# Kernel tuning notes

Measured on AMD Instinct MI355X. Metric: run time of the kernel, lower is better.

The kernel has to match this reference:

```python
import jax, jax.numpy as jnp
import numpy as np

B = 32768
N_TABLES = 26
N_ROWS = 200000
D = 64
N_DENSE = 13
NUM_PAIRS = (N_TABLES + 1) * N_TABLES // 2  # 351, pairs j < i over 27 vectors


def setup_inputs() -> dict:
    key = jax.random.key(0)
    ks = jax.random.split(key, 16)
    def lin(kw, kb, m, n):
        W = jax.random.normal(kw, (m, n), jnp.float32) * np.sqrt(2.0 / (m + n))
        b = jax.random.normal(kb, (m,), jnp.float32) * np.sqrt(1.0 / m)
        return W, b
    bw0, bb0 = lin(ks[0], ks[1], 512, N_DENSE)
    bw1, bb1 = lin(ks[2], ks[3], 256, 512)
    bw2, bb2 = lin(ks[4], ks[5], D, 256)
    tw0, tb0 = lin(ks[6], ks[7], 512, D + NUM_PAIRS)
    tw1, tb1 = lin(ks[8], ks[9], 256, 512)
    tw2, tb2 = lin(ks[10], ks[11], 1, 256)
    bound = np.sqrt(1.0 / N_ROWS)
    emb_tables = jax.random.uniform(ks[12], (N_TABLES, N_ROWS, D), jnp.float32,
                                    minval=-bound, maxval=bound)
    dense_x = jax.random.uniform(ks[13], (B, N_DENSE), jnp.float32)
    indices = jax.random.randint(ks[14], (N_TABLES, B), 0, N_ROWS, jnp.int64)
    return {"dense_x": dense_x, "indices": indices, "emb_tables": emb_tables,
            "bw0": bw0, "bb0": bb0, "bw1": bw1, "bb1": bb1, "bw2": bw2, "bb2": bb2,
            "tw0": tw0, "tb0": tb0, "tw1": tw1, "tb1": tb1, "tw2": tw2, "tb2": tb2}


def reference(dense_x, indices, emb_tables,
              bw0, bb0, bw1, bb1, bw2, bb2,
              tw0, tb0, tw1, tb1, tw2, tb2):
    # bottom MLP (all ReLU, sigmoid_bot = -1)
    h = jax.nn.relu(dense_x @ bw0.T + bb0)
    h = jax.nn.relu(h @ bw1.T + bb1)
    x_bot = jax.nn.relu(h @ bw2.T + bb2)          # [B, D]

    # multi-table EmbeddingBag(sum) with single-index bags -> plain gather
    embs = jax.vmap(lambda tbl, idx: tbl[idx])(emb_tables, indices)  # [26, B, D]

    # dot interaction over 27 feature vectors
    T = jnp.concatenate([x_bot[None], embs], axis=0).transpose(1, 0, 2)  # [B, 27, D]
    Z = jnp.einsum('bnd,bmd->bnm', T, T)                                 # [B, 27, 27]
    li, lj = jnp.tril_indices(N_TABLES + 1, k=-1)  # pairs with j < i (no self)
    Zflat = Z[:, li, lj]                           # [B, 351]
    R = jnp.concatenate([x_bot, Zflat], axis=1)    # [B, 415]

    # top MLP: ReLU, ReLU, Sigmoid (sigmoid_top = 2)
    h = jax.nn.relu(R @ tw0.T + tb0)
    h = jax.nn.relu(h @ tw1.T + tb1)
    p = jax.nn.sigmoid(h @ tw2.T + tb2)            # [B, 1]
    return p
```

## Files before the change

### kernel.cpp

```cpp
#include <hip/hip_runtime.h>
#include <cstddef>
#include <cstdint>

#define B_SZ    32768
#define NTAB    26
#define NROWS   200000

typedef __attribute__((ext_vector_type(8))) short short8v;
typedef __attribute__((ext_vector_type(4))) float f32x4;
typedef __attribute__((ext_vector_type(16))) float f32x16;

__device__ __forceinline__ ushort f2bf(float f) {
    uint32_t u = __builtin_bit_cast(uint32_t, f);
    u += 0x7FFFu + ((u >> 16) & 1u);
    return (ushort)(u >> 16);
}
__device__ __forceinline__ void stage16(const ushort* g, ushort* l) {
    __builtin_amdgcn_global_load_lds(
        (const __attribute__((address_space(1))) unsigned int*)g,
        (__attribute__((address_space(3))) unsigned int*)l, 16, 0, 0);
}
__device__ __forceinline__ void wait_stage_then_barrier(bool last) {
    if (last) asm volatile("s_waitcnt vmcnt(0)" ::: "memory");
    else      asm volatile("s_waitcnt vmcnt(4)" ::: "memory");
    __builtin_amdgcn_sched_barrier(0);
    __builtin_amdgcn_s_barrier();
    __builtin_amdgcn_sched_barrier(0);
}
__device__ __forceinline__ void reads_done_barrier() {
    __builtin_amdgcn_sched_barrier(0);
    __builtin_amdgcn_s_barrier();
    __builtin_amdgcn_sched_barrier(0);
}

__global__ __launch_bounds__(256) void conv_all_k(
    const float* __restrict__ dense_x, const float* __restrict__ bw0,
    const float* __restrict__ tw0, const float* __restrict__ bw1,
    const float* __restrict__ bw2, const float* __restrict__ tw1,
    ushort* __restrict__ dense_pad, ushort* __restrict__ bw0p,
    ushort* __restrict__ tw0p, ushort* __restrict__ bw1c,
    ushort* __restrict__ bw2c, ushort* __restrict__ tw1c)
{
    const int gid = blockIdx.x * 256 + threadIdx.x;
    if (gid < 1048576) {
        int r = gid >> 5, k = gid & 31;
        dense_pad[gid] = (k < 13) ? f2bf(dense_x[r * 13 + k]) : (ushort)0;
    } else if (gid < 1064960) {
        int i = gid - 1048576; int r = i >> 5, k = i & 31;
        bw0p[i] = (k < 13) ? f2bf(bw0[r * 13 + k]) : (ushort)0;
    } else if (gid < 1277952) {
        int i = gid - 1064960; int r = i / 416, k = i - r * 416;
        tw0p[i] = (k < 415) ? f2bf(tw0[r * 415 + k]) : (ushort)0;
    } else if (gid < 1409024) {
        int i = gid - 1277952; bw1c[i] = f2bf(bw1[i]);
    } else if (gid < 1425408) {
        int i = gid - 1409024; bw2c[i] = f2bf(bw2[i]);
    } else if (gid < 1556480) {
        int i = gid - 1425408; tw1c[i] = f2bf(tw1[i]);
    }
}

__global__ __launch_bounds__(256, 2) void fused_k(
    const ushort* __restrict__ dense_pad, const ushort* __restrict__ bw0p,
    const float* __restrict__ bb0, const ushort* __restrict__ bw1c,
    const float* __restrict__ bb1, const ushort* __restrict__ bw2c,
    const float* __restrict__ bb2,
    const float* __restrict__ emb, const int* __restrict__ indices,
    const ushort* __restrict__ tw0p, const float* __restrict__ tb0,
    const ushort* __restrict__ tw1c, const float* __restrict__ tb1,
    const float* __restrict__ tw2, const float* __restrict__ tb2,
    float* __restrict__ out)
{
    __shared__ __align__(16) ushort R1[32 * 512];
    __shared__ __align__(16) ushort Wst[2][256 * 32];
    __shared__ __align__(16) ushort R3[32 * 256];
    ushort* const Wf = &Wst[0][0];
    const int t = threadIdx.x;
    const int lane = t & 63, w = t >> 6;
    const int fr = lane & 15, j16 = lane >> 4;
    const int bBase = blockIdx.x * 32;

    int ir0, ir1, ir2, ir3;
    ir0 = indices[(size_t)(t >> 5) * B_SZ + bBase + (t & 31)];
    ir1 = indices[(size_t)((256 + t) >> 5) * B_SZ + bBase + ((256 + t) & 31)];
    ir2 = indices[(size_t)((512 + t) >> 5) * B_SZ + bBase + ((512 + t) & 31)];
    ir3 = (t < 64) ? indices[(size_t)((768 + t) >> 5) * B_SZ + bBase + ((768 + t) & 31)] : 0;

    if (t < 128) {
        const int r = t >> 2, u = t & 3, us = u ^ ((r >> 1) & 3);
        stage16(dense_pad + (size_t)(bBase + r) * 32 + us * 8, &R3[t * 8]);
    }
#pragma unroll
    for (int i = 0; i < 4; ++i) {
        const int idx = i * 256 + t;
        const int r = idx >> 2, u = idx & 3, us = u ^ ((r >> 1) & 3);
        stage16(bw0p + (size_t)r * 32 + us * 8, &Wst[0][idx * 8]);
        stage16(bw0p + (size_t)(256 + r) * 32 + us * 8, &Wst[1][idx * 8]);
    }
    __syncthreads();

    f32x4 acc0[2][2][4] = {};
    {
        short8v a[2];
#pragma unroll
        for (int m = 0; m < 2; ++m) {
            const int r = m * 16 + fr;
            a[m] = *(const short8v*)&R3[r * 32 + (j16 ^ ((r >> 1) & 3)) * 8];
        }
#pragma unroll
        for (int hh = 0; hh < 2; ++hh) {
            short8v b[4];
#pragma unroll
            for (int n = 0; n < 4; ++n) {
                const int lr = w * 64 + n * 16 + fr;
                b[n] = *(const short8v*)&Wst[hh][lr * 32 + (j16 ^ ((lr >> 1) & 3)) * 8];
            }
            __builtin_amdgcn_s_setprio(1);
#pragma unroll
            for (int m = 0; m < 2; ++m)
#pragma unroll
                for (int n = 0; n < 4; ++n)
                    acc0[hh][m][n] = __builtin_amdgcn_mfma_f32_16x16x32_bf16(b[n], a[m], acc0[hh][m][n], 0, 0, 0);
            __builtin_amdgcn_s_setprio(0);
        }
    }
    __syncthreads();

#pragma unroll
    for (int i = 0; i < 4; ++i) {
        const int idx = i * 256 + t;
        const int r = idx >> 2, u = idx & 3, us = u ^ ((r >> 1) & 3);
        stage16(bw1c + (size_t)r * 512 + us * 8, &Wst[0][idx * 8]);
        stage16(bw1c + (size_t)r * 512 + 32 + us * 8, &Wst[1][idx * 8]);
    }
#pragma unroll
    for (int hh = 0; hh < 2; ++hh)
#pragma unroll
    for (int n = 0; n < 4; ++n) {
        const int ch = hh * 256 + w * 64 + n * 16 + j16 * 4;
        const float4 bv = *(const float4*)&bb0[ch];
#pragma unroll
        for (int m = 0; m < 2; ++m) {
            const int s = m * 16 + fr;
            ushort4 o;
            o.x = f2bf(fmaxf(acc0[hh][m][n][0] + bv.x, 0.f));
            o.y = f2bf(fmaxf(acc0[hh][m][n][1] + bv.y, 0.f));
            o.z = f2bf(fmaxf(acc0[hh][m][n][2] + bv.z, 0.f));
            o.w = f2bf(fmaxf(acc0[hh][m][n][3] + bv.w, 0.f));
            const int u = ch >> 3, su = u ^ (s & 7);
            *(ushort4*)&R1[s * 512 + su * 8 + (ch & 7)] = o;
        }
    }
    __syncthreads();

    f32x4 acc1[2][4] = {};
    for (int st = 0; st < 16; ++st) {
        wait_stage_then_barrier(st == 15);
        const int kt = st * 32;
        short8v a[2], b[4];
#pragma unroll
        for (int m = 0; m < 2; ++m) {
            const int s = m * 16 + fr;
            const int u = (kt >> 3) + j16, su = u ^ (s & 7);
            a[m] = *(const short8v*)&R1[s * 512 + su * 8];
        }
#pragma unroll
        for (int n = 0; n < 4; ++n) {
            const int lr = w * 64 + n * 16 + fr;
            b[n] = *(const short8v*)&Wst[st & 1][lr * 32 + (j16 ^ ((lr >> 1) & 3)) * 8];
        }
        __builtin_amdgcn_s_setprio(1);
#pragma unroll
        for (int m = 0; m < 2; ++m)
#pragma unroll
            for (int n = 0; n < 4; ++n)
                acc1[m][n] = __builtin_amdgcn_mfma_f32_16x16x32_bf16(b[n], a[m], acc1[m][n], 0, 0, 0);
        __builtin_amdgcn_s_setprio(0);
        reads_done_barrier();
        if (st + 2 < 16) {
            const int kt2 = (st + 2) * 32;
#pragma unroll
            for (int i = 0; i < 4; ++i) {
                const int idx = i * 256 + t;
                const int r = idx >> 2, u = idx & 3, us = u ^ ((r >> 1) & 3);
                stage16(bw1c + (size_t)r * 512 + kt2 + us * 8, &Wst[st & 1][idx * 8]);
            }
        }
    }
#pragma unroll
    for (int i = 0; i < 8; ++i) {
        const int idx = i * 256 + t;
        const int st = idx >> 8, within = idx & 255;
        const int r = within >> 2, u = within & 3, us = u ^ ((r >> 1) & 3);
        stage16(bw2c + (size_t)r * 256 + st * 32 + us * 8, &Wf[idx * 8]);
    }
#pragma unroll
    for (int n = 0; n < 4; ++n) {
        const int ch = w * 64 + n * 16 + j16 * 4;
        const float4 bv = *(const float4*)&bb1[ch];
#pragma unroll
        for (int m = 0; m < 2; ++m) {
            const int s = m * 16 + fr;
            ushort4 o;
            o.x = f2bf(fmaxf(acc1[m][n][0] + bv.x, 0.f));
            o.y = f2bf(fmaxf(acc1[m][n][1] + bv.y, 0.f));
            o.z = f2bf(fmaxf(acc1[m][n][2] + bv.z, 0.f));
            o.w = f2bf(fmaxf(acc1[m][n][3] + bv.w, 0.f));
            const int u = ch >> 3, su = u ^ (s & 7);
            *(ushort4*)&R3[s * 256 + su * 8 + (ch & 7)] = o;
        }
    }
    __syncthreads();

    f32x4 acc2[2] = {};
    for (int kt = 0; kt < 256; kt += 32) {
        short8v a[2], b;
#pragma unroll
        for (int m = 0; m < 2; ++m) {
            const int s = m * 16 + fr;
            const int u = (kt >> 3) + j16, su = u ^ (s & 7);
            a[m] = *(const short8v*)&R3[s * 256 + su * 8];
        }
        {
            const int lr = w * 16 + fr;
            b = *(const short8v*)&Wf[(kt >> 5) * 2048 + lr * 32 + (j16 ^ ((lr >> 1) & 3)) * 8];
        }
#pragma unroll
        for (int m = 0; m < 2; ++m)
            acc2[m] = __builtin_amdgcn_mfma_f32_16x16x32_bf16(b, a[m], acc2[m], 0, 0, 0);
    }
    __syncthreads();

#pragma unroll
    for (int i = 0; i < 4; ++i) {
        const int idx = i * 256 + t;
        const int r = idx >> 2, u = idx & 3, us = u ^ ((r >> 1) & 3);
        stage16(tw0p + (size_t)r * 416 + us * 8, &Wst[0][idx * 8]);
        stage16(tw0p + (size_t)(256 + r) * 416 + us * 8, &Wst[1][idx * 8]);
    }
    {
        const int ch = w * 16 + j16 * 4;
        const float4 bv = *(const float4*)&bb2[ch];
#pragma unroll
        for (int m = 0; m < 2; ++m) {
            const int s = m * 16 + fr;
            ushort4 o;
            o.x = f2bf(fmaxf(acc2[m][0] + bv.x, 0.f));
            o.y = f2bf(fmaxf(acc2[m][1] + bv.y, 0.f));
            o.z = f2bf(fmaxf(acc2[m][2] + bv.z, 0.f));
            o.w = f2bf(fmaxf(acc2[m][3] + bv.w, 0.f));
            *(ushort4*)&R1[s * 424 + ch] = o;
        }
    }
    if (t < 32) R1[t * 424 + 415] = 0;
    {
        int* sc = (int*)R3;
        sc[t] = ir0; sc[256 + t] = ir1; sc[512 + t] = ir2;
        if (t < 64) sc[768 + t] = ir3;
    }
    __syncthreads();

    {
        const int* sc = (const int*)R3;
        const int r32 = lane & 31, half = lane >> 5;
        const bool isEmb = (r32 >= 1) && (r32 <= 26);
        const size_t tblOfs = isEmb ? (size_t)(r32 - 1) * NROWS : 0;

#define LOADRAW(dst, s_) { \
        const int idxv = isEmb ? sc[(r32 - 1) * 32 + (s_)] : 0; \
        const float* rp = emb + (tblOfs + (size_t)idxv) * 64 + half * 8; \
        _Pragma("unroll") \
        for (int kq = 0; kq < 4; ++kq) { \
            dst[2 * kq]     = *(const f32x4*)&rp[kq * 16]; \
            dst[2 * kq + 1] = *(const f32x4*)&rp[kq * 16 + 4]; } }

#define COMPUTE(raw, s_) { \
        short8v tf[4]; \
        _Pragma("unroll") \
        for (int kq = 0; kq < 4; ++kq) { \
            short8v v; \
            v[0] = (short)f2bf(raw[2 * kq][0]);     v[1] = (short)f2bf(raw[2 * kq][1]); \
            v[2] = (short)f2bf(raw[2 * kq][2]);     v[3] = (short)f2bf(raw[2 * kq][3]); \
            v[4] = (short)f2bf(raw[2 * kq + 1][0]); v[5] = (short)f2bf(raw[2 * kq + 1][1]); \
            v[6] = (short)f2bf(raw[2 * kq + 1][2]); v[7] = (short)f2bf(raw[2 * kq + 1][3]); \
            if (r32 == 0) v = *(const short8v*)&R1[(s_) * 424 + kq * 16 + half * 8]; \
            else if (!isEmb) v = (short8v)0; \
            tf[kq] = v; } \
        f32x16 c = {}; \
        _Pragma("unroll") \
        for (int kq = 0; kq < 4; ++kq) \
            c = __builtin_amdgcn_mfma_f32_32x32x16_bf16(tf[kq], tf[kq], c, 0, 0, 0); \
        _Pragma("unroll") \
        for (int reg = 0; reg < 16; ++reg) { \
            const int r = (reg & 3) + 8 * (reg >> 2) + 4 * half; \
            if (r < 27 && r32 < r) \
                R1[(s_) * 424 + 64 + (r * (r - 1)) / 2 + r32] = f2bf(c[reg]); } }

        f32x4 rawA[8], rawB[8];
        LOADRAW(rawA, w);
#pragma unroll
        for (int p = 0; p < 4; ++p) {
            const int sA = p * 8 + w;
            const int sB = p * 8 + 4 + w;
            LOADRAW(rawB, sB);
            COMPUTE(rawA, sA);
            if (p < 3) LOADRAW(rawA, p * 8 + 8 + w);
            COMPUTE(rawB, sB);
        }
#undef LOADRAW
#undef COMPUTE
    }
    __syncthreads();

    f32x4 accA[2][2][4] = {};
    for (int st = 0; st < 26; ++st) {
        wait_stage_then_barrier(st == 25);
        const int kt = (st >> 1) * 32, hh = st & 1;
        short8v a[2], b[4];
#pragma unroll
        for (int m = 0; m < 2; ++m) {
            const int s = m * 16 + fr;
            a[m] = *(const short8v*)&R1[s * 424 + ((kt >> 3) + j16) * 8];
        }
#pragma unroll
        for (int n = 0; n < 4; ++n) {
            const int lr = w * 64 + n * 16 + fr;
            b[n] = *(const short8v*)&Wst[st & 1][lr * 32 + (j16 ^ ((lr >> 1) & 3)) * 8];
        }
        __builtin_amdgcn_s_setprio(1);
#pragma unroll
        for (int m = 0; m < 2; ++m)
#pragma unroll
            for (int n = 0; n < 4; ++n)
                accA[hh][m][n] = __builtin_amdgcn_mfma_f32_16x16x32_bf16(b[n], a[m], accA[hh][m][n], 0, 0, 0);
        __builtin_amdgcn_s_setprio(0);
        reads_done_barrier();
        if (st + 2 < 26) {
            const int st2 = st + 2;
            const int kt2 = (st2 >> 1) * 32, hh2 = st2 & 1;
#pragma unroll
            for (int i = 0; i < 4; ++i) {
                const int idx = i * 256 + t;
                const int r = idx >> 2, u = idx & 3, us = u ^ ((r >> 1) & 3);
                stage16(tw0p + (size_t)(hh2 * 256 + r) * 416 + kt2 + us * 8, &Wst[st & 1][idx * 8]);
            }
        }
    }
#pragma unroll
    for (int i = 0; i < 4; ++i) {
        const int idx = i * 256 + t;
        const int r = idx >> 2, u = idx & 3, us = u ^ ((r >> 1) & 3);
        stage16(tw1c + (size_t)r * 512 + us * 8, &Wst[0][idx * 8]);
        stage16(tw1c + (size_t)r * 512 + 32 + us * 8, &Wst[1][idx * 8]);
    }
#pragma unroll
    for (int hh = 0; hh < 2; ++hh)
#pragma unroll
    for (int n = 0; n < 4; ++n) {
        const int ch = hh * 256 + w * 64 + n * 16 + j16 * 4;
        const float4 bv = *(const float4*)&tb0[ch];
#pragma unroll
        for (int m = 0; m < 2; ++m) {
            const int s = m * 16 + fr;
            ushort4 o;
            o.x = f2bf(fmaxf(accA[hh][m][n][0] + bv.x, 0.f));
            o.y = f2bf(fmaxf(accA[hh][m][n][1] + bv.y, 0.f));
            o.z = f2bf(fmaxf(accA[hh][m][n][2] + bv.z, 0.f));
            o.w = f2bf(fmaxf(accA[hh][m][n][3] + bv.w, 0.f));
            const int u = ch >> 3, su = u ^ (s & 7);
            *(ushort4*)&R1[s * 512 + su * 8 + (ch & 7)] = o;
        }
    }
    __syncthreads();

    f32x4 accB[2][4] = {};
    for (int st = 0; st < 16; ++st) {
        wait_stage_then_barrier(st == 15);
        const int kt = st * 32;
        short8v a[2], b[4];
#pragma unroll
        for (int m = 0; m < 2; ++m) {
            const int s = m * 16 + fr;
            const int u = (kt >> 3) + j16, su = u ^ (s & 7);
            a[m] = *(const short8v*)&R1[s * 512 + su * 8];
        }
#pragma unroll
        for (int n = 0; n < 4; ++n) {
            const int lr = w * 64 + n * 16 + fr;
            b[n] = *(const short8v*)&Wst[st & 1][lr * 32 + (j16 ^ ((lr >> 1) & 3)) * 8];
        }
        __builtin_amdgcn_s_setprio(1);
#pragma unroll
        for (int m = 0; m < 2; ++m)
#pragma unroll
            for (int n = 0; n < 4; ++n)
                accB[m][n] = __builtin_amdgcn_mfma_f32_16x16x32_bf16(b[n], a[m], accB[m][n], 0, 0, 0);
        __builtin_amdgcn_s_setprio(0);
        reads_done_barrier();
        if (st + 2 < 16) {
            const int kt2 = (st + 2) * 32;
#pragma unroll
            for (int i = 0; i < 4; ++i) {
                const int idx = i * 256 + t;
                const int r = idx >> 2, u = idx & 3, us = u ^ ((r >> 1) & 3);
                stage16(tw1c + (size_t)r * 512 + kt2 + us * 8, &Wst[st & 1][idx * 8]);
            }
        }
    }

    float* red = (float*)R3;
    float part[2] = {0.f, 0.f};
#pragma unroll
    for (int n = 0; n < 4; ++n) {
        const int ch = w * 64 + n * 16 + j16 * 4;
        const float4 bv = *(const float4*)&tb1[ch];
        const float4 wv = *(const float4*)&tw2[ch];
#pragma unroll
        for (int m = 0; m < 2; ++m) {
            part[m] += fmaxf(accB[m][n][0] + bv.x, 0.f) * wv.x
                     + fmaxf(accB[m][n][1] + bv.y, 0.f) * wv.y
                     + fmaxf(accB[m][n][2] + bv.z, 0.f) * wv.z
                     + fmaxf(accB[m][n][3] + bv.w, 0.f) * wv.w;
        }
    }
#pragma unroll
    for (int m = 0; m < 2; ++m) {
        float v = part[m];
        v += __shfl_xor(v, 16, 64);
        v += __shfl_xor(v, 32, 64);
        if (lane < 16) red[w * 32 + m * 16 + fr] = v;
    }
    __syncthreads();
    if (t < 32) {
        const float sm = red[t] + red[32 + t] + red[64 + t] + red[96 + t];
        out[bBase + t] = 1.f / (1.f + expf(-(sm + tb2[0])));
    }
}

extern "C" void kernel_launch(void* const* d_in, const int* in_sizes, int n_in,
                              void* d_out, int out_size, void* d_ws, size_t ws_size,
                              hipStream_t stream)
{
    (void)in_sizes; (void)n_in; (void)out_size; (void)ws_size;
    const float* dense_x = (const float*)d_in[0];
    const int*   indices = (const int*)d_in[1];
    const float* emb     = (const float*)d_in[2];
    const float* bw0 = (const float*)d_in[3];
    const float* bb0 = (const float*)d_in[4];
    const float* bw1 = (const float*)d_in[5];
    const float* bb1 = (const float*)d_in[6];
    const float* bw2 = (const float*)d_in[7];
    const float* bb2 = (const float*)d_in[8];
    const float* tw0 = (const float*)d_in[9];
    const float* tb0 = (const float*)d_in[10];
    const float* tw1 = (const float*)d_in[11];
    const float* tb1 = (const float*)d_in[12];
    const float* tw2 = (const float*)d_in[13];
    const float* tb2 = (const float*)d_in[14];
    float* out = (float*)d_out;

    ushort* ws16      = (ushort*)d_ws;
    ushort* dense_pad = ws16;
    ushort* bw0p      = dense_pad + (size_t)B_SZ * 32;
    ushort* tw0p      = bw0p + 512 * 32;
    ushort* bw1c      = tw0p + 512 * 416;
    ushort* bw2c      = bw1c + 256 * 512;
    ushort* tw1c      = bw2c + 64 * 256;

    conv_all_k<<<dim3(6080), dim3(256), 0, stream>>>(
        dense_x, bw0, tw0, bw1, bw2, tw1,
        dense_pad, bw0p, tw0p, bw1c, bw2c, tw1c);

    fused_k<<<dim3(B_SZ / 32), dim3(256), 0, stream>>>(
        dense_pad, bw0p, bb0, bw1c, bb1, bw2c, bb2,
        emb, indices, tw0p, tb0, tw1c, tb1, tw2, tb2, out);
}
```

Baseline: 111.5 us.

## Triple-buffer weight staging to drop one barrier per K-step

The double-buffered LDS weight pipelines in the three big GEMM stages become three-slot ring buffers, with R3 as the third slot. Prefetched tiles then never overwrite the slot being read, so the second per-iteration barrier (reads_done) is removed and only one barrier per step remains. The loops are fully unrolled so buffer selection is static, and the index scratch moves from R3 into the tail of R1. The cost is more LDS in use, a larger unrolled code footprint, and a prologue that issues three stages up front while the wait count stays at vmcnt(4).

```diff
diff --git a/kernel.cpp b/kernel.cpp
--- a/kernel.cpp
+++ b/kernel.cpp
@@ -20,14 +20,9 @@
         (const __attribute__((address_space(1))) unsigned int*)g,
         (__attribute__((address_space(3))) unsigned int*)l, 16, 0, 0);
 }
-__device__ __forceinline__ void wait_stage_then_barrier(bool last) {
+__device__ __forceinline__ void pipe_barrier(bool last) {
     if (last) asm volatile("s_waitcnt vmcnt(0)" ::: "memory");
     else      asm volatile("s_waitcnt vmcnt(4)" ::: "memory");
-    __builtin_amdgcn_sched_barrier(0);
-    __builtin_amdgcn_s_barrier();
-    __builtin_amdgcn_sched_barrier(0);
-}
-__device__ __forceinline__ void reads_done_barrier() {
     __builtin_amdgcn_sched_barrier(0);
     __builtin_amdgcn_s_barrier();
     __builtin_amdgcn_sched_barrier(0);
@@ -132,6 +127,7 @@
         const int r = idx >> 2, u = idx & 3, us = u ^ ((r >> 1) & 3);
         stage16(bw1c + (size_t)r * 512 + us * 8, &Wst[0][idx * 8]);
         stage16(bw1c + (size_t)r * 512 + 32 + us * 8, &Wst[1][idx * 8]);
+        stage16(bw1c + (size_t)r * 512 + 64 + us * 8, &R3[idx * 8]);
     }
 #pragma unroll
     for (int hh = 0; hh < 2; ++hh)
@@ -154,9 +150,11 @@
     __syncthreads();
 
     f32x4 acc1[2][4] = {};
+#pragma unroll
     for (int st = 0; st < 16; ++st) {
-        wait_stage_then_barrier(st == 15);
+        pipe_barrier(st == 15);
         const int kt = st * 32;
+        ushort* const bufp = (st % 3 == 0) ? Wst[0] : (st % 3 == 1) ? Wst[1] : R3;
         short8v a[2], b[4];
 #pragma unroll
         for (int m = 0; m < 2; ++m) {
@@ -167,7 +165,7 @@
 #pragma unroll
         for (int n = 0; n < 4; ++n) {
             const int lr = w * 64 + n * 16 + fr;
-            b[n] = *(const short8v*)&Wst[st & 1][lr * 32 + (j16 ^ ((lr >> 1) & 3)) * 8];
+            b[n] = *(const short8v*)&bufp[lr * 32 + (j16 ^ ((lr >> 1) & 3)) * 8];
         }
         __builtin_amdgcn_s_setprio(1);
 #pragma unroll
@@ -176,17 +174,20 @@
             for (int n = 0; n < 4; ++n)
                 acc1[m][n] = __builtin_amdgcn_mfma_f32_16x16x32_bf16(b[n], a[m], acc1[m][n], 0, 0, 0);
         __builtin_amdgcn_s_setprio(0);
-        reads_done_barrier();
-        if (st + 2 < 16) {
-            const int kt2 = (st + 2) * 32;
+        if (st >= 1 && st <= 13) {
+            const int st2 = st + 2;
+            const int kt2 = st2 * 32;
+            ushort* const dstp = (st2 % 3 == 0) ? Wst[0] : (st2 % 3 == 1) ? Wst[1] : R3;
 #pragma unroll
             for (int i = 0; i < 4; ++i) {
                 const int idx = i * 256 + t;
                 const int r = idx >> 2, u = idx & 3, us = u ^ ((r >> 1) & 3);
-                stage16(bw1c + (size_t)r * 512 + kt2 + us * 8, &Wst[st & 1][idx * 8]);
+                stage16(bw1c + (size_t)r * 512 + kt2 + us * 8, &dstp[idx * 8]);
             }
         }
     }
+    __syncthreads();
+
 #pragma unroll
     for (int i = 0; i < 8; ++i) {
         const int idx = i * 256 + t;
@@ -237,6 +238,7 @@
         const int r = idx >> 2, u = idx & 3, us = u ^ ((r >> 1) & 3);
         stage16(tw0p + (size_t)r * 416 + us * 8, &Wst[0][idx * 8]);
         stage16(tw0p + (size_t)(256 + r) * 416 + us * 8, &Wst[1][idx * 8]);
+        stage16(tw0p + (size_t)r * 416 + 32 + us * 8, &R3[idx * 8]);
     }
     {
         const int ch = w * 16 + j16 * 4;
@@ -254,14 +256,14 @@
     }
     if (t < 32) R1[t * 424 + 415] = 0;
     {
-        int* sc = (int*)R3;
+        int* sc = (int*)&R1[32 * 424];
         sc[t] = ir0; sc[256 + t] = ir1; sc[512 + t] = ir2;
         if (t < 64) sc[768 + t] = ir3;
     }
     __syncthreads();
 
     {
-        const int* sc = (const int*)R3;
+        const int* sc = (const int*)&R1[32 * 424];
         const int r32 = lane & 31, half = lane >> 5;
         const bool isEmb = (r32 >= 1) && (r32 <= 26);
         const size_t tblOfs = isEmb ? (size_t)(r32 - 1) * NROWS : 0;
@@ -313,9 +315,11 @@
     __syncthreads();
 
     f32x4 accA[2][2][4] = {};
+#pragma unroll
     for (int st = 0; st < 26; ++st) {
-        wait_stage_then_barrier(st == 25);
+        pipe_barrier(st == 25);
         const int kt = (st >> 1) * 32, hh = st & 1;
+        ushort* const bufp = (st % 3 == 0) ? Wst[0] : (st % 3 == 1) ? Wst[1] : R3;
         short8v a[2], b[4];
 #pragma unroll
         for (int m = 0; m < 2; ++m) {
@@ -325,7 +329,7 @@
 #pragma unroll
         for (int n = 0; n < 4; ++n) {
             const int lr = w * 64 + n * 16 + fr;
-            b[n] = *(const short8v*)&Wst[st & 1][lr * 32 + (j16 ^ ((lr >> 1) & 3)) * 8];
+            b[n] = *(const short8v*)&bufp[lr * 32 + (j16 ^ ((lr >> 1) & 3)) * 8];
         }
         __builtin_amdgcn_s_setprio(1);
 #pragma unroll
@@ -334,24 +338,27 @@
             for (int n = 0; n < 4; ++n)
                 accA[hh][m][n] = __builtin_amdgcn_mfma_f32_16x16x32_bf16(b[n], a[m], accA[hh][m][n], 0, 0, 0);
         __builtin_amdgcn_s_setprio(0);
-        reads_done_barrier();
-        if (st + 2 < 26) {
+        if (st >= 1 && st <= 23) {
             const int st2 = st + 2;
             const int kt2 = (st2 >> 1) * 32, hh2 = st2 & 1;
+            ushort* const dstp = (st2 % 3 == 0) ? Wst[0] : (st2 % 3 == 1) ? Wst[1] : R3;
 #pragma unroll
             for (int i = 0; i < 4; ++i) {
                 const int idx = i * 256 + t;
                 const int r = idx >> 2, u = idx & 3, us = u ^ ((r >> 1) & 3);
-                stage16(tw0p + (size_t)(hh2 * 256 + r) * 416 + kt2 + us * 8, &Wst[st & 1][idx * 8]);
+                stage16(tw0p + (size_t)(hh2 * 256 + r) * 416 + kt2 + us * 8, &dstp[idx * 8]);
             }
         }
     }
+    __syncthreads();
+
 #pragma unroll
     for (int i = 0; i < 4; ++i) {
         const int idx = i * 256 + t;
         const int r = idx >> 2, u = idx & 3, us = u ^ ((r >> 1) & 3);
         stage16(tw1c + (size_t)r * 512 + us * 8, &Wst[0][idx * 8]);
         stage16(tw1c + (size_t)r * 512 + 32 + us * 8, &Wst[1][idx * 8]);
+        stage16(tw1c + (size_t)r * 512 + 64 + us * 8, &R3[idx * 8]);
     }
 #pragma unroll
     for (int hh = 0; hh < 2; ++hh)
@@ -374,9 +381,11 @@
     __syncthreads();
 
     f32x4 accB[2][4] = {};
+#pragma unroll
     for (int st = 0; st < 16; ++st) {
-        wait_stage_then_barrier(st == 15);
+        pipe_barrier(st == 15);
         const int kt = st * 32;
+        ushort* const bufp = (st % 3 == 0) ? Wst[0] : (st % 3 == 1) ? Wst[1] : R3;
         short8v a[2], b[4];
 #pragma unroll
         for (int m = 0; m < 2; ++m) {
@@ -387,7 +396,7 @@
 #pragma unroll
         for (int n = 0; n < 4; ++n) {
             const int lr = w * 64 + n * 16 + fr;
-            b[n] = *(const short8v*)&Wst[st & 1][lr * 32 + (j16 ^ ((lr >> 1) & 3)) * 8];
+            b[n] = *(const short8v*)&bufp[lr * 32 + (j16 ^ ((lr >> 1) & 3)) * 8];
         }
         __builtin_amdgcn_s_setprio(1);
 #pragma unroll
@@ -396,17 +405,19 @@
             for (int n = 0; n < 4; ++n)
                 accB[m][n] = __builtin_amdgcn_mfma_f32_16x16x32_bf16(b[n], a[m], accB[m][n], 0, 0, 0);
         __builtin_amdgcn_s_setprio(0);
-        reads_done_barrier();
-        if (st + 2 < 16) {
-            const int kt2 = (st + 2) * 32;
+        if (st >= 1 && st <= 13) {
+            const int st2 = st + 2;
+            const int kt2 = st2 * 32;
+            ushort* const dstp = (st2 % 3 == 0) ? Wst[0] : (st2 % 3 == 1) ? Wst[1] : R3;
 #pragma unroll
             for (int i = 0; i < 4; ++i) {
                 const int idx = i * 256 + t;
                 const int r = idx >> 2, u = idx & 3, us = u ^ ((r >> 1) & 3);
-                stage16(tw1c + (size_t)r * 512 + kt2 + us * 8, &Wst[st & 1][idx * 8]);
+                stage16(tw1c + (size_t)r * 512 + kt2 + us * 8, &dstp[idx * 8]);
             }
         }
     }
+    __syncthreads();
 
     float* red = (float*)R3;
     float part[2] = {0.f, 0.f};
```

Result: no change. 109.7 us (-1.6%).
